# Optimization experiments

Hardware: AMD Instinct MI355X
Metric: run time of the kernel (lower is better)

The kernel has to match this reference:

```python
import jax, jax.numpy as jnp
import numpy as np

NUM_SITES_X = 2048
NUM_SITES_Y = 4096
NUM_CLB_SITES = 6_000_000
NUM_SLICE_SITES = 6_000_000
NUM_SITES = NUM_SITES_X * NUM_SITES_Y  # global flattened site-id space


def setup_inputs() -> dict:
    key = jax.random.key(0)
    k1, k2, k3, k4 = jax.random.split(key, 4)
    # CLB slice site ids (x*num_sites_y + y), sorted as produced from the column-major fabric scan
    slice_sites = jnp.sort(
        jax.random.randint(k1, (NUM_SLICE_SITES,), 0, NUM_SITES, dtype=jnp.int32))
    # per-CLB-site signature count; >0 means the site already has instances committed
    site_det_sig_idx = jax.random.randint(
        k2, (NUM_CLB_SITES,), 0, 4, dtype=jnp.int32)
    # compact CLB address -> global site id map (monotone by construction in the original)
    addr2site_map = jnp.sort(
        jax.random.randint(k3, (NUM_CLB_SITES,), 0, NUM_SITES, dtype=jnp.int32))
    # per-slice-site legalization score (site_det_score analogue)
    site_scores = jax.random.normal(k4, (NUM_SLICE_SITES,), dtype=jnp.float32)
    return {
        "slice_sites": slice_sites,
        "site_det_sig_idx": site_det_sig_idx,
        "addr2site_map": addr2site_map,
        "site_scores": site_scores,
    }


def _remaining_mask(slice_sites, site_det_sig_idx, addr2site_map):
    """Faithful jit-friendly version of compute_remaining_slice_sites.

    torch/np original:
      assigned = addr2site_map[site_det_sig_idx > 0]
      mask[np.in1d(slice_sites, assigned)] = True; return ~mask
    We avoid the data-dependent boolean gather by replacing unassigned
    entries with a -1 sentinel (site ids are >= 0), sorting, and doing a
    vectorized membership test via searchsorted.
    """
    n = addr2site_map.shape[0]
    assigned = jnp.where(site_det_sig_idx > 0, addr2site_map, jnp.int32(-1))
    assigned_sorted = jnp.sort(assigned)  # sentinels land at the front
    pos = jnp.searchsorted(assigned_sorted, slice_sites, side="left")
    pos = jnp.clip(pos, 0, n - 1)
    found = assigned_sorted[pos] == slice_sites  # in1d membership
    return ~found  # True where the slice site is still available


def reference(slice_sites, site_det_sig_idx, addr2site_map, site_scores):
    remaining = _remaining_mask(slice_sites, site_det_sig_idx, addr2site_map)
    # scores of still-available candidate sites (zeros where already assigned)
    avail_scores = jnp.where(remaining, site_scores, jnp.zeros((), site_scores.dtype))
    return remaining, avail_scores
```

## Files before the change

kernel.cpp:

```cpp
#include <hip/hip_runtime.h>


typedef int   v4i __attribute__((ext_vector_type(4)));
typedef float v4f __attribute__((ext_vector_type(4)));

static constexpr int WORDS_PER_BIN = 128;
static constexpr int SITES_PER_BIN = 4096;
static constexpr int BIN_SHIFT     = 12;
static constexpr int NBINS         = 2048;
static constexpr int BLOCK         = 256;

__global__ __launch_bounds__(BLOCK) void bounds_kernel(
    const int* __restrict__ a2s, int* __restrict__ eb, int n_clb)
{
    const int t = blockIdx.x * BLOCK + threadIdx.x;
    const int s = t * 4;
    if (s >= n_clb) return;
    int v[4];
    int cnt;
    if (s + 4 <= n_clb) {
        v4i a = __builtin_nontemporal_load((const v4i*)(a2s + s));
        v[0] = a.x; v[1] = a.y; v[2] = a.z; v[3] = a.w;
        cnt = 4;
    } else {
        cnt = n_clb - s;
        for (int j = 0; j < cnt; ++j) v[j] = a2s[s + j];
    }
    int pbin = (s == 0) ? -1 : (a2s[s - 1] >> BIN_SHIFT);
    for (int j = 0; j < cnt; ++j) {
        const int i = s + j;
        const int cbin = v[j] >> BIN_SHIFT;
        for (int b = pbin + 1; b <= cbin; ++b) eb[b] = i;
        if (i == n_clb - 1)
            for (int b = cbin + 1; b <= NBINS; ++b) eb[b] = n_clb;
        pbin = cbin;
    }
}

__global__ __launch_bounds__(BLOCK) void mark_kernel(
    const int* __restrict__ sig, const int* __restrict__ a2s,
    const int* __restrict__ eb, unsigned int* __restrict__ bm, int n_clb)
{
    __shared__ unsigned int lbm[WORDS_PER_BIN];

    const int g        = blockIdx.x;
    const int siteBase = g * SITES_PER_BIN;
    const int siteEnd  = siteBase + SITES_PER_BIN;

    if (threadIdx.x < WORDS_PER_BIN) lbm[threadIdx.x] = 0u;
    const int e0 = eb[g], e1 = eb[g + 1];
    __syncthreads();

    const int mstart = e0 & ~3;
    for (int s = mstart + threadIdx.x * 8; s < e1; s += BLOCK * 8) {
        int av[8], gv[8];
        if (s + 8 <= n_clb) {
            v4i a0 = __builtin_nontemporal_load((const v4i*)(a2s + s));
            v4i a1 = __builtin_nontemporal_load((const v4i*)(a2s + s + 4));
            v4i g0 = __builtin_nontemporal_load((const v4i*)(sig + s));
            v4i g1 = __builtin_nontemporal_load((const v4i*)(sig + s + 4));
            av[0]=a0.x; av[1]=a0.y; av[2]=a0.z; av[3]=a0.w;
            av[4]=a1.x; av[5]=a1.y; av[6]=a1.z; av[7]=a1.w;
            gv[0]=g0.x; gv[1]=g0.y; gv[2]=g0.z; gv[3]=g0.w;
            gv[4]=g1.x; gv[5]=g1.y; gv[6]=g1.z; gv[7]=g1.w;
        } else {
#pragma unroll
            for (int j = 0; j < 8; ++j) {
                const int i = s + j;
                const bool ok = i < n_clb;
                av[j] = ok ? a2s[i] : -1;
                gv[j] = ok ? sig[i] : 0;
            }
        }
        unsigned int curw = 0xFFFFFFFFu, curm = 0u;
#pragma unroll
        for (int j = 0; j < 8; ++j) {
            const int site = av[j];
            if (gv[j] > 0 && site >= siteBase && site < siteEnd) {
                const unsigned int u = (unsigned int)(site - siteBase);
                const unsigned int w = u >> 5;
                const unsigned int m = 1u << (u & 31u);
                if (w == curw) curm |= m;
                else { if (curm) atomicOr(&lbm[curw], curm); curw = w; curm = m; }
            }
        }
        if (curm) atomicOr(&lbm[curw], curm);
    }

    __syncthreads();

    if (threadIdx.x < WORDS_PER_BIN / 4)
        ((v4i*)(bm + g * WORDS_PER_BIN))[threadIdx.x] =
            ((const v4i*)lbm)[threadIdx.x];
}

__global__ __launch_bounds__(BLOCK) void probe_kernel(
    const int* __restrict__ ss, const float* __restrict__ sc,
    const unsigned int* __restrict__ bm,
    float* __restrict__ rem, float* __restrict__ avail, int n4)
{
    const int q = blockIdx.x * BLOCK + threadIdx.x;
    if (q >= n4) return;
    v4i s = __builtin_nontemporal_load((const v4i*)ss + q);
    v4f f = __builtin_nontemporal_load((const v4f*)sc + q);
    v4f r, a;
#pragma unroll
    for (int j = 0; j < 4; ++j) {
        const unsigned int u   = (unsigned int)s[j];
        const unsigned int bit = (bm[u >> 5] >> (u & 31u)) & 1u;
        r[j] = bit ? 0.0f : 1.0f;
        a[j] = bit ? 0.0f : f[j];
    }
    __builtin_nontemporal_store(r, (v4f*)rem + q);
    __builtin_nontemporal_store(a, (v4f*)avail + q);
}

__global__ void probe_tail_kernel(
    const int* __restrict__ ss, const float* __restrict__ sc,
    const unsigned int* __restrict__ bm,
    float* __restrict__ rem, float* __restrict__ avail, int start, int n)
{
    const int i = start + blockIdx.x * blockDim.x + threadIdx.x;
    if (i >= n) return;
    const unsigned int u   = (unsigned int)ss[i];
    const unsigned int bit = (bm[u >> 5] >> (u & 31u)) & 1u;
    rem[i]   = bit ? 0.0f : 1.0f;
    avail[i] = bit ? 0.0f : sc[i];
}

extern "C" void kernel_launch(void* const* d_in, const int* in_sizes, int n_in,
                              void* d_out, int out_size, void* d_ws, size_t ws_size,
                              hipStream_t stream) {
    const int*   ss  = (const int*)d_in[0];
    const int*   sig = (const int*)d_in[1];
    const int*   a2s = (const int*)d_in[2];
    const float* sc  = (const float*)d_in[3];
    const int n_slice = in_sizes[0];
    const int n_clb   = in_sizes[1];

    unsigned int* bm = (unsigned int*)d_ws;
    int*          eb = (int*)(bm + NBINS * WORDS_PER_BIN);

    const int t1 = (n_clb / 4 + BLOCK - 1) / BLOCK + 1;
    bounds_kernel<<<t1, BLOCK, 0, stream>>>(a2s, eb, n_clb);

    mark_kernel<<<NBINS, BLOCK, 0, stream>>>(sig, a2s, eb, bm, n_clb);

    float* rem   = (float*)d_out;
    float* avail = rem + n_slice;
    const int n4 = n_slice / 4;
    if (n4 > 0)
        probe_kernel<<<(n4 + BLOCK - 1) / BLOCK, BLOCK, 0, stream>>>(
            ss, sc, bm, rem, avail, n4);
    if (n4 * 4 < n_slice)
        probe_tail_kernel<<<1, 64, 0, stream>>>(ss, sc, bm, rem, avail,
                                                n4 * 4, n_slice);
}
```

Before: 144.2 us.

## Fuse bounds, mark and probe into one per-bin kernel using binary search

Replaces the three-kernel pipeline (bin bounds scan, bitmap mark, global probe) with one kernel per 4096-site bin. Each block binary-searches its ranges in both sorted arrays, builds the bin bitmap in shared memory, and probes the slice sites that fall in the same bin. This removes the bounds pass, the global bitmap write and read-back, and two launches. In exchange it relies on slice_sites being sorted, and each block's probe loop runs serially after its mark phase.

Result: no change. 144.9 us (+0.5%).

```diff
diff --git a/kernel.cpp b/kernel.cpp
--- a/kernel.cpp
+++ b/kernel.cpp
@@ -10,46 +10,43 @@
 static constexpr int NBINS         = 2048;
 static constexpr int BLOCK         = 256;
 
-__global__ __launch_bounds__(BLOCK) void bounds_kernel(
-    const int* __restrict__ a2s, int* __restrict__ eb, int n_clb)
+__device__ __forceinline__ int lower_bound_dev(
+    const int* __restrict__ a, int n, int key)
 {
-    const int t = blockIdx.x * BLOCK + threadIdx.x;
-    const int s = t * 4;
-    if (s >= n_clb) return;
-    int v[4];
-    int cnt;
-    if (s + 4 <= n_clb) {
-        v4i a = __builtin_nontemporal_load((const v4i*)(a2s + s));
-        v[0] = a.x; v[1] = a.y; v[2] = a.z; v[3] = a.w;
-        cnt = 4;
-    } else {
-        cnt = n_clb - s;
-        for (int j = 0; j < cnt; ++j) v[j] = a2s[s + j];
+    int lo = 0, hi = n;
+    while (lo < hi) {
+        const int mid = (lo + hi) >> 1;
+        if (a[mid] < key) lo = mid + 1; else hi = mid;
     }
-    int pbin = (s == 0) ? -1 : (a2s[s - 1] >> BIN_SHIFT);
-    for (int j = 0; j < cnt; ++j) {
-        const int i = s + j;
-        const int cbin = v[j] >> BIN_SHIFT;
-        for (int b = pbin + 1; b <= cbin; ++b) eb[b] = i;
-        if (i == n_clb - 1)
-            for (int b = cbin + 1; b <= NBINS; ++b) eb[b] = n_clb;
-        pbin = cbin;
-    }
+    return lo;
 }
 
-__global__ __launch_bounds__(BLOCK) void mark_kernel(
-    const int* __restrict__ sig, const int* __restrict__ a2s,
-    const int* __restrict__ eb, unsigned int* __restrict__ bm, int n_clb)
+__global__ __launch_bounds__(BLOCK) void fused_kernel(
+    const int* __restrict__ ss, const int* __restrict__ sig,
+    const int* __restrict__ a2s, const float* __restrict__ sc,
+    float* __restrict__ rem, float* __restrict__ avail,
+    int n_clb, int n_slice)
 {
     __shared__ unsigned int lbm[WORDS_PER_BIN];
+    __shared__ int sb[4];
 
     const int g        = blockIdx.x;
-    const int siteBase = g * SITES_PER_BIN;
+    const int siteBase = g << BIN_SHIFT;
     const int siteEnd  = siteBase + SITES_PER_BIN;
 
     if (threadIdx.x < WORDS_PER_BIN) lbm[threadIdx.x] = 0u;
-    const int e0 = eb[g], e1 = eb[g + 1];
+
+    if ((threadIdx.x & 63) == 0) {
+        const int w = threadIdx.x >> 6;
+        int r;
+        if      (w == 0) r = lower_bound_dev(a2s, n_clb,   siteBase);
+        else if (w == 1) r = lower_bound_dev(a2s, n_clb,   siteEnd);
+        else if (w == 2) r = lower_bound_dev(ss,  n_slice, siteBase);
+        else             r = lower_bound_dev(ss,  n_slice, siteEnd);
+        sb[w] = r;
+    }
     __syncthreads();
+    const int e0 = sb[0], e1 = sb[1], f0 = sb[2], f1 = sb[3];
 
     const int mstart = e0 & ~3;
     for (int s = mstart + threadIdx.x * 8; s < e1; s += BLOCK * 8) {
@@ -89,43 +86,45 @@
 
     __syncthreads();
 
-    if (threadIdx.x < WORDS_PER_BIN / 4)
-        ((v4i*)(bm + g * WORDS_PER_BIN))[threadIdx.x] =
-            ((const v4i*)lbm)[threadIdx.x];
-}
+    const int fa = (f0 + 3) & ~3;
+    const int fb = f1 & ~3;
+    const int head_end = fa < f1 ? fa : f1;
 
-__global__ __launch_bounds__(BLOCK) void probe_kernel(
-    const int* __restrict__ ss, const float* __restrict__ sc,
-    const unsigned int* __restrict__ bm,
-    float* __restrict__ rem, float* __restrict__ avail, int n4)
-{
-    const int q = blockIdx.x * BLOCK + threadIdx.x;
-    if (q >= n4) return;
-    v4i s = __builtin_nontemporal_load((const v4i*)ss + q);
-    v4f f = __builtin_nontemporal_load((const v4f*)sc + q);
-    v4f r, a;
+    {
+        const int i = f0 + (int)threadIdx.x;
+        if (i < head_end) {
+            const unsigned int u   = (unsigned int)(ss[i] - siteBase);
+            const unsigned int bit = (lbm[u >> 5] >> (u & 31u)) & 1u;
+            rem[i]   = bit ? 0.0f : 1.0f;
+            avail[i] = bit ? 0.0f : sc[i];
+        }
+    }
+    if (fa < fb) {
+        for (int q = fa / 4 + (int)threadIdx.x; q < fb / 4; q += BLOCK) {
+            v4i s = __builtin_nontemporal_load((const v4i*)ss + q);
+            v4f f = __builtin_nontemporal_load((const v4f*)sc + q);
+            v4f r, a;
 #pragma unroll
-    for (int j = 0; j < 4; ++j) {
-        const unsigned int u   = (unsigned int)s[j];
-        const unsigned int bit = (bm[u >> 5] >> (u & 31u)) & 1u;
-        r[j] = bit ? 0.0f : 1.0f;
-        a[j] = bit ? 0.0f : f[j];
+            for (int j = 0; j < 4; ++j) {
+                const unsigned int u   = (unsigned int)(s[j] - siteBase);
+                const unsigned int bit = (lbm[u >> 5] >> (u & 31u)) & 1u;
+                r[j] = bit ? 0.0f : 1.0f;
+                a[j] = bit ? 0.0f : f[j];
+            }
+            __builtin_nontemporal_store(r, (v4f*)rem + q);
+            __builtin_nontemporal_store(a, (v4f*)avail + q);
+        }
     }
-    __builtin_nontemporal_store(r, (v4f*)rem + q);
-    __builtin_nontemporal_store(a, (v4f*)avail + q);
-}
-
-__global__ void probe_tail_kernel(
-    const int* __restrict__ ss, const float* __restrict__ sc,
-    const unsigned int* __restrict__ bm,
-    float* __restrict__ rem, float* __restrict__ avail, int start, int n)
-{
-    const int i = start + blockIdx.x * blockDim.x + threadIdx.x;
-    if (i >= n) return;
-    const unsigned int u   = (unsigned int)ss[i];
-    const unsigned int bit = (bm[u >> 5] >> (u & 31u)) & 1u;
-    rem[i]   = bit ? 0.0f : 1.0f;
-    avail[i] = bit ? 0.0f : sc[i];
+    {
+        const int tstart = fb > head_end ? fb : head_end;
+        const int i = tstart + (int)threadIdx.x;
+        if (i < f1) {
+            const unsigned int u   = (unsigned int)(ss[i] - siteBase);
+            const unsigned int bit = (lbm[u >> 5] >> (u & 31u)) & 1u;
+            rem[i]   = bit ? 0.0f : 1.0f;
+            avail[i] = bit ? 0.0f : sc[i];
+        }
+    }
 }
 
 extern "C" void kernel_launch(void* const* d_in, const int* in_sizes, int n_in,
@@ -138,21 +137,9 @@
     const int n_slice = in_sizes[0];
     const int n_clb   = in_sizes[1];
 
-    unsigned int* bm = (unsigned int*)d_ws;
-    int*          eb = (int*)(bm + NBINS * WORDS_PER_BIN);
-
-    const int t1 = (n_clb / 4 + BLOCK - 1) / BLOCK + 1;
-    bounds_kernel<<<t1, BLOCK, 0, stream>>>(a2s, eb, n_clb);
-
-    mark_kernel<<<NBINS, BLOCK, 0, stream>>>(sig, a2s, eb, bm, n_clb);
-
     float* rem   = (float*)d_out;
     float* avail = rem + n_slice;
-    const int n4 = n_slice / 4;
-    if (n4 > 0)
-        probe_kernel<<<(n4 + BLOCK - 1) / BLOCK, BLOCK, 0, stream>>>(
-            ss, sc, bm, rem, avail, n4);
-    if (n4 * 4 < n_slice)
-        probe_tail_kernel<<<1, 64, 0, stream>>>(ss, sc, bm, rem, avail,
-                                                n4 * 4, n_slice);
+
+    fused_kernel<<<NBINS, BLOCK, 0, stream>>>(ss, sig, a2s, sc, rem, avail,
+                                              n_clb, n_slice);
 }
```

## Replace binned shared-memory bitmap build with memset plus global atomicOr marking

Applied to the files above, without the earlier changes.

The per-bin bounds kernel and the per-bin shared-memory bitmap construction are removed. The bitmap is now zeroed with hipMemsetAsync, and a flat mark kernel, with 16 entries per thread, ORs bits into the global bitmap with global atomics. The tail-probe kernel is folded into the main probe kernel, cutting launches from four to three (memset plus two kernels). This drops the bounds pass and the bin scheduling but relies on global atomics to a 1 MB bitmap and no longer exploits the sorted order for shared-memory locality.

Result: slower. 147.8 us (+2.5%).

```diff
diff --git a/kernel.cpp b/kernel.cpp
--- a/kernel.cpp
+++ b/kernel.cpp
@@ -4,128 +4,79 @@
 typedef int   v4i __attribute__((ext_vector_type(4)));
 typedef float v4f __attribute__((ext_vector_type(4)));
 
-static constexpr int WORDS_PER_BIN = 128;
-static constexpr int SITES_PER_BIN = 4096;
-static constexpr int BIN_SHIFT     = 12;
-static constexpr int NBINS         = 2048;
-static constexpr int BLOCK         = 256;
-
-__global__ __launch_bounds__(BLOCK) void bounds_kernel(
-    const int* __restrict__ a2s, int* __restrict__ eb, int n_clb)
-{
-    const int t = blockIdx.x * BLOCK + threadIdx.x;
-    const int s = t * 4;
-    if (s >= n_clb) return;
-    int v[4];
-    int cnt;
-    if (s + 4 <= n_clb) {
-        v4i a = __builtin_nontemporal_load((const v4i*)(a2s + s));
-        v[0] = a.x; v[1] = a.y; v[2] = a.z; v[3] = a.w;
-        cnt = 4;
-    } else {
-        cnt = n_clb - s;
-        for (int j = 0; j < cnt; ++j) v[j] = a2s[s + j];
-    }
-    int pbin = (s == 0) ? -1 : (a2s[s - 1] >> BIN_SHIFT);
-    for (int j = 0; j < cnt; ++j) {
-        const int i = s + j;
-        const int cbin = v[j] >> BIN_SHIFT;
-        for (int b = pbin + 1; b <= cbin; ++b) eb[b] = i;
-        if (i == n_clb - 1)
-            for (int b = cbin + 1; b <= NBINS; ++b) eb[b] = n_clb;
-        pbin = cbin;
-    }
-}
+static constexpr int BLOCK  = 256;
+static constexpr int MPT    = 16;
+static constexpr int NSITES = 1 << 23;
+static constexpr int NWORDS = NSITES / 32;
 
 __global__ __launch_bounds__(BLOCK) void mark_kernel(
     const int* __restrict__ sig, const int* __restrict__ a2s,
-    const int* __restrict__ eb, unsigned int* __restrict__ bm, int n_clb)
+    unsigned int* __restrict__ bm, int n_clb)
 {
-    __shared__ unsigned int lbm[WORDS_PER_BIN];
+    const int s = (blockIdx.x * BLOCK + threadIdx.x) * MPT;
+    if (s >= n_clb) return;
 
-    const int g        = blockIdx.x;
-    const int siteBase = g * SITES_PER_BIN;
-    const int siteEnd  = siteBase + SITES_PER_BIN;
-
-    if (threadIdx.x < WORDS_PER_BIN) lbm[threadIdx.x] = 0u;
-    const int e0 = eb[g], e1 = eb[g + 1];
-    __syncthreads();
-
-    const int mstart = e0 & ~3;
-    for (int s = mstart + threadIdx.x * 8; s < e1; s += BLOCK * 8) {
-        int av[8], gv[8];
-        if (s + 8 <= n_clb) {
-            v4i a0 = __builtin_nontemporal_load((const v4i*)(a2s + s));
-            v4i a1 = __builtin_nontemporal_load((const v4i*)(a2s + s + 4));
-            v4i g0 = __builtin_nontemporal_load((const v4i*)(sig + s));
-            v4i g1 = __builtin_nontemporal_load((const v4i*)(sig + s + 4));
-            av[0]=a0.x; av[1]=a0.y; av[2]=a0.z; av[3]=a0.w;
-            av[4]=a1.x; av[5]=a1.y; av[6]=a1.z; av[7]=a1.w;
-            gv[0]=g0.x; gv[1]=g0.y; gv[2]=g0.z; gv[3]=g0.w;
-            gv[4]=g1.x; gv[5]=g1.y; gv[6]=g1.z; gv[7]=g1.w;
-        } else {
+    int av[MPT], gv[MPT];
+    if (s + MPT <= n_clb) {
 #pragma unroll
-            for (int j = 0; j < 8; ++j) {
-                const int i = s + j;
-                const bool ok = i < n_clb;
-                av[j] = ok ? a2s[i] : -1;
-                gv[j] = ok ? sig[i] : 0;
-            }
+        for (int k = 0; k < MPT / 4; ++k) {
+            v4i a = __builtin_nontemporal_load((const v4i*)(a2s + s + 4 * k));
+            v4i g = __builtin_nontemporal_load((const v4i*)(sig + s + 4 * k));
+            av[4*k+0] = a.x; av[4*k+1] = a.y; av[4*k+2] = a.z; av[4*k+3] = a.w;
+            gv[4*k+0] = g.x; gv[4*k+1] = g.y; gv[4*k+2] = g.z; gv[4*k+3] = g.w;
         }
-        unsigned int curw = 0xFFFFFFFFu, curm = 0u;
+    } else {
 #pragma unroll
-        for (int j = 0; j < 8; ++j) {
-            const int site = av[j];
-            if (gv[j] > 0 && site >= siteBase && site < siteEnd) {
-                const unsigned int u = (unsigned int)(site - siteBase);
-                const unsigned int w = u >> 5;
-                const unsigned int m = 1u << (u & 31u);
-                if (w == curw) curm |= m;
-                else { if (curm) atomicOr(&lbm[curw], curm); curw = w; curm = m; }
-            }
+        for (int j = 0; j < MPT; ++j) {
+            const int i = s + j;
+            const bool ok = i < n_clb;
+            av[j] = ok ? a2s[i] : -1;
+            gv[j] = ok ? sig[i] : 0;
         }
-        if (curm) atomicOr(&lbm[curw], curm);
     }
 
-    __syncthreads();
-
-    if (threadIdx.x < WORDS_PER_BIN / 4)
-        ((v4i*)(bm + g * WORDS_PER_BIN))[threadIdx.x] =
-            ((const v4i*)lbm)[threadIdx.x];
+    unsigned int curw = 0xFFFFFFFFu, curm = 0u;
+#pragma unroll
+    for (int j = 0; j < MPT; ++j) {
+        if (gv[j] > 0) {
+            const unsigned int u = (unsigned int)av[j];
+            const unsigned int w = u >> 5;
+            const unsigned int m = 1u << (u & 31u);
+            if (w == curw) curm |= m;
+            else { if (curm) atomicOr(&bm[curw], curm); curw = w; curm = m; }
+        }
+    }
+    if (curm) atomicOr(&bm[curw], curm);
 }
 
 __global__ __launch_bounds__(BLOCK) void probe_kernel(
     const int* __restrict__ ss, const float* __restrict__ sc,
     const unsigned int* __restrict__ bm,
-    float* __restrict__ rem, float* __restrict__ avail, int n4)
+    float* __restrict__ rem, float* __restrict__ avail,
+    int n4, int n_slice)
 {
     const int q = blockIdx.x * BLOCK + threadIdx.x;
-    if (q >= n4) return;
-    v4i s = __builtin_nontemporal_load((const v4i*)ss + q);
-    v4f f = __builtin_nontemporal_load((const v4f*)sc + q);
-    v4f r, a;
+    if (q < n4) {
+        v4i s = __builtin_nontemporal_load((const v4i*)ss + q);
+        v4f f = __builtin_nontemporal_load((const v4f*)sc + q);
+        v4f r, a;
 #pragma unroll
-    for (int j = 0; j < 4; ++j) {
-        const unsigned int u   = (unsigned int)s[j];
-        const unsigned int bit = (bm[u >> 5] >> (u & 31u)) & 1u;
-        r[j] = bit ? 0.0f : 1.0f;
-        a[j] = bit ? 0.0f : f[j];
+        for (int j = 0; j < 4; ++j) {
+            const unsigned int u   = (unsigned int)s[j];
+            const unsigned int bit = (bm[u >> 5] >> (u & 31u)) & 1u;
+            r[j] = bit ? 0.0f : 1.0f;
+            a[j] = bit ? 0.0f : f[j];
+        }
+        __builtin_nontemporal_store(r, (v4f*)rem + q);
+        __builtin_nontemporal_store(a, (v4f*)avail + q);
+    } else if (q == n4) {
+        for (int i = n4 * 4; i < n_slice; ++i) {
+            const unsigned int u   = (unsigned int)ss[i];
+            const unsigned int bit = (bm[u >> 5] >> (u & 31u)) & 1u;
+            rem[i]   = bit ? 0.0f : 1.0f;
+            avail[i] = bit ? 0.0f : sc[i];
+        }
     }
-    __builtin_nontemporal_store(r, (v4f*)rem + q);
-    __builtin_nontemporal_store(a, (v4f*)avail + q);
-}
-
-__global__ void probe_tail_kernel(
-    const int* __restrict__ ss, const float* __restrict__ sc,
-    const unsigned int* __restrict__ bm,
-    float* __restrict__ rem, float* __restrict__ avail, int start, int n)
-{
-    const int i = start + blockIdx.x * blockDim.x + threadIdx.x;
-    if (i >= n) return;
-    const unsigned int u   = (unsigned int)ss[i];
-    const unsigned int bit = (bm[u >> 5] >> (u & 31u)) & 1u;
-    rem[i]   = bit ? 0.0f : 1.0f;
-    avail[i] = bit ? 0.0f : sc[i];
 }
 
 extern "C" void kernel_launch(void* const* d_in, const int* in_sizes, int n_in,
@@ -139,20 +90,15 @@
     const int n_clb   = in_sizes[1];
 
     unsigned int* bm = (unsigned int*)d_ws;
-    int*          eb = (int*)(bm + NBINS * WORDS_PER_BIN);
 
-    const int t1 = (n_clb / 4 + BLOCK - 1) / BLOCK + 1;
-    bounds_kernel<<<t1, BLOCK, 0, stream>>>(a2s, eb, n_clb);
+    hipMemsetAsync(bm, 0, NWORDS * sizeof(unsigned int), stream);
 
-    mark_kernel<<<NBINS, BLOCK, 0, stream>>>(sig, a2s, eb, bm, n_clb);
+    const int mb = (n_clb + BLOCK * MPT - 1) / (BLOCK * MPT);
+    mark_kernel<<<mb, BLOCK, 0, stream>>>(sig, a2s, bm, n_clb);
 
     float* rem   = (float*)d_out;
     float* avail = rem + n_slice;
     const int n4 = n_slice / 4;
-    if (n4 > 0)
-        probe_kernel<<<(n4 + BLOCK - 1) / BLOCK, BLOCK, 0, stream>>>(
-            ss, sc, bm, rem, avail, n4);
-    if (n4 * 4 < n_slice)
-        probe_tail_kernel<<<1, 64, 0, stream>>>(ss, sc, bm, rem, avail,
-                                                n4 * 4, n_slice);
+    const int pb = (n4 + 1 + BLOCK - 1) / BLOCK;
+    probe_kernel<<<pb, BLOCK, 0, stream>>>(ss, sc, bm, rem, avail, n4, n_slice);
 }
```
